# Kernel optimization log

Measured on AMD Instinct MI355X. Metric: run time of the kernel, lower is better.

Reference implementation:

```python
import jax, jax.numpy as jnp
import numpy as np

B, L, H = 32, 2048, 512
EPS = 1e-6


def setup_inputs() -> dict:
    key = jax.random.key(0)
    k1, k2 = jax.random.split(key)
    hidden = jax.random.normal(k1, (B, L, H), dtype=jnp.float32)
    # nn.Linear(H, H): weight [H, H], bias [H]; use kaiming-uniform-like scale
    bound = 1.0 / np.sqrt(H)
    W = jax.random.uniform(k2, (H, H), dtype=jnp.float32, minval=-bound, maxval=bound)
    b = jnp.zeros((H,), dtype=jnp.float32)
    return {"hidden": hidden, "W": W, "b": b}


def reference(hidden, W, b):
    Bn, Ln, Hn = hidden.shape

    def step(M, k):
        # k: [B, H]; key == value == hidden[:, t, :]
        v_pred = jnp.einsum("bij,bj->bi", M, k)               # M @ k
        denom = jnp.sum(k * k, axis=-1, keepdims=True) + EPS   # [B, 1]
        delta_v = k - v_pred / denom                           # v - v_pred/denom (v == k)
        M = M + jnp.einsum("bi,bj->bij", delta_v, k)           # outer-product update
        return M, None

    M0 = jnp.zeros((Bn, Hn, Hn), dtype=hidden.dtype)
    xs = jnp.swapaxes(hidden[:, :-1, :], 0, 1)  # [L-1, B, H]
    M, _ = jax.lax.scan(step, M0, xs)

    query = hidden[:, -1, :]                                   # [B, H]
    context = jnp.einsum("bij,bj->bi", M, query)               # [B, H]
    return context @ W.T + b                                   # read_proj
```

## Files before the change

### kernel.cpp

```cpp
#include <hip/hip_runtime.h>

#define B_  32
#define L_  2048
#define H_  512
#define T_  2047
#define CA  32
#define NC  64
#define EPSF 1e-6f

template <int CTRL>
__device__ __forceinline__ float dpp_shift_add(float x) {
  int t = __builtin_amdgcn_update_dpp(0, __float_as_int(x), CTRL, 0xf, 0xf, true);
  return x + __int_as_float(t);
}
__device__ __forceinline__ float wave_reduce_lane63(float x) {
  x = dpp_shift_add<0x111>(x);
  x = dpp_shift_add<0x112>(x);
  x = dpp_shift_add<0x114>(x);
  x = dpp_shift_add<0x118>(x);
  x = dpp_shift_add<0x142>(x);
  x = dpp_shift_add<0x143>(x);
  return x;
}

__device__ __forceinline__ void load_lds16(const float* g, float* l) {
  __builtin_amdgcn_global_load_lds(
      (const __attribute__((address_space(1))) unsigned int*)(g),
      (__attribute__((address_space(3))) unsigned int*)(l), 16, 0, 0);
}

__global__ __launch_bounds__(256) void
deltarule_gram(const float* __restrict__ hidden,
               float* __restrict__ tmT, float* __restrict__ dvec) {
  const int cb = blockIdx.x, b = blockIdx.y;
  const int tid = threadIdx.x, lane = tid & 63, wv = tid >> 6;
  __shared__ __align__(16) float Kc[CA * H_];
  __shared__ float G[CA * 33];

  const float* kb = hidden + ((size_t)b * L_ + (size_t)cb * CA) * H_;
#pragma unroll
  for (int u = 0; u < 16; ++u) {
    const int off = (u * 4 + wv) * 256;
    load_lds16(kb + off + 4 * lane, &Kc[off]);
  }
  __asm__ volatile("s_waitcnt vmcnt(0)" ::: "memory");
  __syncthreads();
  if (cb == NC - 1) {
    if (tid < 128) *(float4*)&Kc[31 * H_ + 4 * tid] = make_float4(0.f, 0.f, 0.f, 0.f);
    __syncthreads();
  }

  float kr[8][8];
#pragma unroll
  for (int i = 0; i < 8; ++i) {
    const int r = 8 * wv + i;
    *(float4*)&kr[i][0] = *(const float4*)&Kc[r * H_ + 4 * lane];
    *(float4*)&kr[i][4] = *(const float4*)&Kc[r * H_ + 256 + 4 * lane];
  }
  float g[8] = {0.f, 0.f, 0.f, 0.f, 0.f, 0.f, 0.f, 0.f};
  for (int j = 8 * wv; j < CA; ++j) {
    float kj[8];
    *(float4*)&kj[0] = *(const float4*)&Kc[j * H_ + 4 * lane];
    *(float4*)&kj[4] = *(const float4*)&Kc[j * H_ + 256 + 4 * lane];
#pragma unroll
    for (int i = 0; i < 8; ++i) {
      float p = kr[i][0] * kj[0];
#pragma unroll
      for (int u = 1; u < 8; ++u) p = fmaf(kr[i][u], kj[u], p);
      p = wave_reduce_lane63(p);
      float s = __int_as_float(__builtin_amdgcn_readlane(__float_as_int(p), 63));
      g[i] = (lane == j) ? s : g[i];
    }
  }
  if (lane < CA) {
#pragma unroll
    for (int i = 0; i < 8; ++i) G[(8 * wv + i) * 33 + lane] = g[i];
  }
  __syncthreads();

  if (wv == 0) {
    const int j = lane & 31;
    float X[CA];
#pragma unroll
    for (int t = CA - 1; t >= 0; --t) {
      float inner = 0.f;
#pragma unroll
      for (int s = t + 1; s < CA; ++s) inner = fmaf(G[t * 33 + s], X[s], inner);
      X[t] = (((j == t) ? 1.f : 0.f) - inner) / (G[t * 33 + t] + EPSF);
    }
    if (lane < CA) {
      const size_t base = ((size_t)b * NC + cb) * (CA * CA);
#pragma unroll
      for (int u = 0; u < 8; ++u)
        *(float4*)&tmT[base + j * CA + 4 * u] =
            make_float4(X[4 * u], X[4 * u + 1], X[4 * u + 2], X[4 * u + 3]);
      dvec[((size_t)b * NC + cb) * CA + lane] = G[j * 33 + j] + EPSF;
    }
  }
}

__global__ __launch_bounds__(512) void
deltarule_scan(const float* __restrict__ hidden,
               const float* __restrict__ Wm, const float* __restrict__ bias,
               const float* __restrict__ tmT, const float* __restrict__ dvec,
               float* __restrict__ out) {
  const int b = blockIdx.x, tid = threadIdx.x, lane = tid & 63, wv = tid >> 6;
  __shared__ __align__(16) float Kc[2][CA * H_];
  __shared__ float Tm[CA * 33];
  __shared__ float Dv[CA];
  __shared__ float Yv[CA];
  __shared__ float2 SigS[CA];
  __shared__ __align__(16) float Wv[H_];
  __shared__ __align__(16) float Ctx[H_];

  const float* hb = hidden + (size_t)b * L_ * H_;
  float wh = hb[(size_t)(L_ - 1) * H_ + tid];
  Wv[tid] = wh;
  float ch = 0.f;

  {
    const float* kb = hb + (size_t)(NC - 1) * CA * H_;
#pragma unroll
    for (int u = 0; u < 8; ++u) {
      const int off = (u * 8 + wv) * 256;
      load_lds16(kb + off + 4 * lane, &Kc[1][off]);
    }
    const size_t tb = (size_t)b * NC + (NC - 1);
    float2 t2 = *(const float2*)&tmT[tb * (CA * CA) + 2 * tid];
    const int e0 = 2 * tid;
    Tm[(e0 >> 5) * 33 + (e0 & 31)] = t2.x;
    Tm[((e0 + 1) >> 5) * 33 + ((e0 + 1) & 31)] = t2.y;
    if (tid < CA) Dv[tid] = dvec[tb * CA + tid];
  }
  __asm__ volatile("s_waitcnt vmcnt(0)" ::: "memory");
  __syncthreads();
  if (tid < 128) *(float4*)&Kc[1][31 * H_ + 4 * tid] = make_float4(0.f, 0.f, 0.f, 0.f);
  __syncthreads();

  for (int c = NC - 1; c >= 0; --c) {
    const int buf = c & 1;

    float2 tmN = make_float2(0.f, 0.f); float dN = 0.f;
    if (c > 0) {
      const size_t tb = (size_t)b * NC + (c - 1);
      tmN = *(const float2*)&tmT[tb * (CA * CA) + 2 * tid];
      if (tid < CA) dN = dvec[tb * CA + tid];
      const float* kb = hb + (size_t)(c - 1) * CA * H_;
#pragma unroll
      for (int u = 0; u < 8; ++u) {
        const int off = (u * 8 + wv) * 256;
        load_lds16(kb + off + 4 * lane, &Kc[buf ^ 1][off]);
      }
    }

    {
      float4 wa = *(const float4*)&Wv[4 * lane];
      float4 wb = *(const float4*)&Wv[256 + 4 * lane];
#pragma unroll
      for (int i = 0; i < 4; ++i) {
        const int r = 4 * wv + i;
        float4 ka = *(const float4*)&Kc[buf][r * H_ + 4 * lane];
        float4 kc = *(const float4*)&Kc[buf][r * H_ + 256 + 4 * lane];
        float p = ka.x * wa.x;
        p = fmaf(ka.y, wa.y, p); p = fmaf(ka.z, wa.z, p); p = fmaf(ka.w, wa.w, p);
        p = fmaf(kc.x, wb.x, p); p = fmaf(kc.y, wb.y, p);
        p = fmaf(kc.z, wb.z, p); p = fmaf(kc.w, wb.w, p);
        p = wave_reduce_lane63(p);
        if (lane == 63) Yv[r] = p;
      }
    }
    __syncthreads();

    if (wv == 0) {
      const int j = lane & 31, hf = lane >> 5;
      float sig = 0.f;
#pragma unroll
      for (int s0 = 0; s0 < 16; ++s0) {
        const int s = hf * 16 + s0;
        sig = fmaf(Tm[s * 33 + j], Yv[s], sig);
      }
      sig += __shfl_down(sig, 32);
      if (lane < CA) SigS[j] = make_float2(sig, Dv[j] * sig);
    }
    __syncthreads();

    if (c > 0) {
      const int e0 = 2 * tid;
      Tm[(e0 >> 5) * 33 + (e0 & 31)] = tmN.x;
      Tm[((e0 + 1) >> 5) * 33 + ((e0 + 1) & 31)] = tmN.y;
      if (tid < CA) Dv[tid] = dN;
    }

#pragma unroll
    for (int t = 0; t < CA; ++t) {
      float2 ss = SigS[t];
      float kvv = Kc[buf][t * H_ + tid];
      wh = fmaf(-ss.x, kvv, wh);
      ch = fmaf(ss.y, kvv, ch);
    }
    Wv[tid] = wh;
    __asm__ volatile("s_waitcnt vmcnt(0)" ::: "memory");
    __syncthreads();
  }

  Ctx[tid] = ch;
  __syncthreads();
  float acc = bias[tid];
  const float* wr = Wm + (size_t)tid * H_;
#pragma unroll 8
  for (int i = 0; i < H_; i += 4) {
    float4 w4 = *(const float4*)(wr + i);
    float4 cv = *(const float4*)&Ctx[i];
    acc = fmaf(w4.x, cv.x, acc); acc = fmaf(w4.y, cv.y, acc);
    acc = fmaf(w4.z, cv.z, acc); acc = fmaf(w4.w, cv.w, acc);
  }
  out[(size_t)b * H_ + tid] = acc;
}

extern "C" void kernel_launch(void* const* d_in, const int* in_sizes, int n_in,
                              void* d_out, int out_size, void* d_ws, size_t ws_size,
                              hipStream_t stream) {
  const float* hidden = (const float*)d_in[0];
  const float* Wm     = (const float*)d_in[1];
  const float* bias   = (const float*)d_in[2];
  float* out = (float*)d_out;

  float* tmT  = (float*)d_ws;
  float* dvec = tmT + (size_t)B_ * NC * CA * CA;

  dim3 gridA(NC, B_);
  deltarule_gram<<<gridA, 256, 0, stream>>>(hidden, tmT, dvec);
  deltarule_scan<<<B_, 512, 0, stream>>>(hidden, Wm, bias, tmT, dvec, out);
}
```

Measured before the change: 386.3 us.

## Stage keys as fp16 copy and triple-buffer the chunked delta-rule scan

```diff
diff --git a/kernel.cpp b/kernel.cpp
--- a/kernel.cpp
+++ b/kernel.cpp
@@ -1,4 +1,5 @@
 #include <hip/hip_runtime.h>
+#include <hip/hip_fp16.h>
 
 #define B_  32
 #define L_  2048
@@ -28,10 +29,16 @@
       (const __attribute__((address_space(1))) unsigned int*)(g),
       (__attribute__((address_space(3))) unsigned int*)(l), 16, 0, 0);
 }
+__device__ __forceinline__ void load_lds16h(const unsigned short* g, unsigned short* l) {
+  __builtin_amdgcn_global_load_lds(
+      (const __attribute__((address_space(1))) unsigned int*)(g),
+      (__attribute__((address_space(3))) unsigned int*)(l), 16, 0, 0);
+}
 
 __global__ __launch_bounds__(256) void
 deltarule_gram(const float* __restrict__ hidden,
-               float* __restrict__ tmT, float* __restrict__ dvec) {
+               float* __restrict__ tmT, float* __restrict__ dvec,
+               unsigned short* __restrict__ Kh) {
   const int cb = blockIdx.x, b = blockIdx.y;
   const int tid = threadIdx.x, lane = tid & 63, wv = tid >> 6;
   __shared__ __align__(16) float Kc[CA * H_];
@@ -47,6 +54,19 @@
   __syncthreads();
   if (cb == NC - 1) {
     if (tid < 128) *(float4*)&Kc[31 * H_ + 4 * tid] = make_float4(0.f, 0.f, 0.f, 0.f);
+    __syncthreads();
+  }
+
+  if (Kh) {
+    unsigned int* dst = (unsigned int*)(Kh + ((size_t)b * L_ + (size_t)cb * CA) * H_);
+#pragma unroll
+    for (int u = 0; u < 32; ++u) {
+      const int i = u * 256 + tid;
+      float2 v = *(const float2*)&Kc[2 * i];
+      __half2 h2 = __floats2half2_rn(v.x, v.y);
+      dst[i] = *(const unsigned int*)&h2;
+      *(float2*)&Kc[2 * i] = __half22float2(h2);
+    }
     __syncthreads();
   }
 
@@ -100,10 +120,150 @@
 }
 
 __global__ __launch_bounds__(512) void
-deltarule_scan(const float* __restrict__ hidden,
-               const float* __restrict__ Wm, const float* __restrict__ bias,
-               const float* __restrict__ tmT, const float* __restrict__ dvec,
-               float* __restrict__ out) {
+deltarule_scan_f16(const float* __restrict__ hidden,
+                   const unsigned short* __restrict__ Kh,
+                   const float* __restrict__ Wm, const float* __restrict__ bias,
+                   const float* __restrict__ tmT, const float* __restrict__ dvec,
+                   float* __restrict__ out) {
+  const int b = blockIdx.x, tid = threadIdx.x, lane = tid & 63, wv = tid >> 6;
+  __shared__ __align__(16) unsigned short Kc[3][CA * H_];
+  __shared__ float Tm[2][CA * 33];
+  __shared__ float Yv[CA];
+  __shared__ float2 SigS[CA];
+  __shared__ __align__(16) float Wv[H_];
+  __shared__ __align__(16) float Ctx[H_];
+
+  const float* hb = hidden + (size_t)b * L_ * H_;
+  const unsigned short* kbb = Kh + (size_t)b * L_ * H_;
+
+  float wh = hb[(size_t)(L_ - 1) * H_ + tid];
+  Wv[tid] = wh;
+  float ch = 0.f;
+
+  {
+    const unsigned short* kp = kbb + (size_t)(NC - 1) * CA * H_;
+#pragma unroll
+    for (int u = 0; u < 4; ++u) {
+      const int off = (u * 8 + wv) * 512;
+      load_lds16h(kp + off + 8 * lane, &Kc[(NC - 1) % 3][off]);
+    }
+  }
+  asm volatile("" ::: "memory");
+  const size_t tbP = (size_t)b * NC + (NC - 1);
+  float2 tmR = *(const float2*)&tmT[tbP * (CA * CA) + 2 * tid];
+  float dR = dvec[tbP * CA + (lane & 31)];
+  asm volatile("" ::: "memory");
+  {
+    const unsigned short* kp = kbb + (size_t)(NC - 2) * CA * H_;
+#pragma unroll
+    for (int u = 0; u < 4; ++u) {
+      const int off = (u * 8 + wv) * 512;
+      load_lds16h(kp + off + 8 * lane, &Kc[(NC - 2) % 3][off]);
+    }
+  }
+  asm volatile("" ::: "memory");
+  {
+    const int f0 = 2 * tid;
+    Tm[1][(f0 >> 5) * 33 + (f0 & 31)] = tmR.x;
+    Tm[1][((f0 + 1) >> 5) * 33 + ((f0 + 1) & 31)] = tmR.y;
+  }
+  float dCur = dR;
+  asm volatile("s_waitcnt vmcnt(4) lgkmcnt(0)\n\ts_barrier" ::: "memory");
+
+  for (int c = NC - 1; c >= 0; --c) {
+    const int rb = c % 3;
+
+    if (c >= 1) {
+      const size_t tb = (size_t)b * NC + (c - 1);
+      tmR = *(const float2*)&tmT[tb * (CA * CA) + 2 * tid];
+      dR = dvec[tb * CA + (lane & 31)];
+    }
+    asm volatile("" ::: "memory");
+    if (c >= 2) {
+      const unsigned short* kp = kbb + (size_t)(c - 2) * CA * H_;
+#pragma unroll
+      for (int u = 0; u < 4; ++u) {
+        const int off = (u * 8 + wv) * 512;
+        load_lds16h(kp + off + 8 * lane, &Kc[(c - 2) % 3][off]);
+      }
+    }
+    asm volatile("" ::: "memory");
+
+    {
+      float4 wa = *(const float4*)&Wv[8 * lane];
+      float4 wb2 = *(const float4*)&Wv[8 * lane + 4];
+#pragma unroll
+      for (int i = 0; i < 4; ++i) {
+        const int r = 4 * wv + i;
+        uint4 kw = *(const uint4*)&Kc[rb][r * H_ + 8 * lane];
+        float2 f0 = __half22float2(*(__half2*)&kw.x);
+        float2 f1 = __half22float2(*(__half2*)&kw.y);
+        float2 f2 = __half22float2(*(__half2*)&kw.z);
+        float2 f3 = __half22float2(*(__half2*)&kw.w);
+        float p = f0.x * wa.x;
+        p = fmaf(f0.y, wa.y, p); p = fmaf(f1.x, wa.z, p); p = fmaf(f1.y, wa.w, p);
+        p = fmaf(f2.x, wb2.x, p); p = fmaf(f2.y, wb2.y, p);
+        p = fmaf(f3.x, wb2.z, p); p = fmaf(f3.y, wb2.w, p);
+        p = wave_reduce_lane63(p);
+        if (lane == 63) Yv[r] = p;
+      }
+    }
+    asm volatile("s_waitcnt lgkmcnt(0)\n\ts_barrier" ::: "memory");
+
+    {
+      const int j = lane & 31, hf = lane >> 5;
+      float sig = 0.f;
+#pragma unroll
+      for (int s0 = 0; s0 < 16; ++s0) {
+        const int s = hf * 16 + s0;
+        sig = fmaf(Tm[c & 1][s * 33 + j], Yv[s], sig);
+      }
+      sig += __shfl_xor(sig, 32);
+      float sj = dCur * sig;
+      if (lane < 32) SigS[j] = make_float2(sig, sj);
+    }
+    if (c >= 1) {
+      const int f0 = 2 * tid;
+      Tm[(c - 1) & 1][(f0 >> 5) * 33 + (f0 & 31)] = tmR.x;
+      Tm[(c - 1) & 1][((f0 + 1) >> 5) * 33 + ((f0 + 1) & 31)] = tmR.y;
+      dCur = dR;
+    }
+
+#pragma unroll
+    for (int t = 0; t < CA; ++t) {
+      float2 ss = SigS[t];
+      float kvv = __half2float(*(const __half*)&Kc[rb][t * H_ + tid]);
+      wh = fmaf(-ss.x, kvv, wh);
+      ch = fmaf(ss.y, kvv, ch);
+    }
+    Wv[tid] = wh;
+
+    if (c >= 2) {
+      asm volatile("s_waitcnt vmcnt(4) lgkmcnt(0)\n\ts_barrier" ::: "memory");
+    } else {
+      asm volatile("s_waitcnt vmcnt(0) lgkmcnt(0)\n\ts_barrier" ::: "memory");
+    }
+  }
+
+  Ctx[tid] = ch;
+  __syncthreads();
+  float acc = bias[tid];
+  const float* wr = Wm + (size_t)tid * H_;
+#pragma unroll 8
+  for (int i = 0; i < H_; i += 4) {
+    float4 w4 = *(const float4*)(wr + i);
+    float4 cv = *(const float4*)&Ctx[i];
+    acc = fmaf(w4.x, cv.x, acc); acc = fmaf(w4.y, cv.y, acc);
+    acc = fmaf(w4.z, cv.z, acc); acc = fmaf(w4.w, cv.w, acc);
+  }
+  out[(size_t)b * H_ + tid] = acc;
+}
+
+__global__ __launch_bounds__(512) void
+deltarule_scan_f32(const float* __restrict__ hidden,
+                   const float* __restrict__ Wm, const float* __restrict__ bias,
+                   const float* __restrict__ tmT, const float* __restrict__ dvec,
+                   float* __restrict__ out) {
   const int b = blockIdx.x, tid = threadIdx.x, lane = tid & 63, wv = tid >> 6;
   __shared__ __align__(16) float Kc[2][CA * H_];
   __shared__ float Tm[CA * 33];
@@ -139,7 +299,6 @@
 
   for (int c = NC - 1; c >= 0; --c) {
     const int buf = c & 1;
-
     float2 tmN = make_float2(0.f, 0.f); float dN = 0.f;
     if (c > 0) {
       const size_t tb = (size_t)b * NC + (c - 1);
@@ -152,7 +311,6 @@
         load_lds16(kb + off + 4 * lane, &Kc[buf ^ 1][off]);
       }
     }
-
     {
       float4 wa = *(const float4*)&Wv[4 * lane];
       float4 wb = *(const float4*)&Wv[256 + 4 * lane];
@@ -170,7 +328,6 @@
       }
     }
     __syncthreads();
-
     if (wv == 0) {
       const int j = lane & 31, hf = lane >> 5;
       float sig = 0.f;
@@ -183,14 +340,12 @@
       if (lane < CA) SigS[j] = make_float2(sig, Dv[j] * sig);
     }
     __syncthreads();
-
     if (c > 0) {
       const int e0 = 2 * tid;
       Tm[(e0 >> 5) * 33 + (e0 & 31)] = tmN.x;
       Tm[((e0 + 1) >> 5) * 33 + ((e0 + 1) & 31)] = tmN.y;
       if (tid < CA) Dv[tid] = dN;
     }
-
 #pragma unroll
     for (int t = 0; t < CA; ++t) {
       float2 ss = SigS[t];
@@ -225,10 +380,21 @@
   const float* bias   = (const float*)d_in[2];
   float* out = (float*)d_out;
 
-  float* tmT  = (float*)d_ws;
-  float* dvec = tmT + (size_t)B_ * NC * CA * CA;
+  const size_t szKh = (size_t)B_ * L_ * H_ * sizeof(unsigned short);
+  const size_t szTm = (size_t)B_ * NC * CA * CA * sizeof(float);
+  const size_t szD  = (size_t)B_ * NC * CA * sizeof(float);
 
   dim3 gridA(NC, B_);
-  deltarule_gram<<<gridA, 256, 0, stream>>>(hidden, tmT, dvec);
-  deltarule_scan<<<B_, 512, 0, stream>>>(hidden, Wm, bias, tmT, dvec, out);
-}
+  if (ws_size >= szKh + szTm + szD) {
+    unsigned short* Kh = (unsigned short*)d_ws;
+    float* tmT  = (float*)((char*)d_ws + szKh);
+    float* dvec = tmT + (size_t)B_ * NC * CA * CA;
+    deltarule_gram<<<gridA, 256, 0, stream>>>(hidden, tmT, dvec, Kh);
+    deltarule_scan_f16<<<B_, 512, 0, stream>>>(hidden, Kh, Wm, bias, tmT, dvec, out);
+  } else {
+    float* tmT  = (float*)d_ws;
+    float* dvec = tmT + (size_t)B_ * NC * CA * CA;
+    deltarule_gram<<<gridA, 256, 0, stream>>>(hidden, tmT, dvec, nullptr);
+    deltarule_scan_f32<<<B_, 512, 0, stream>>>(hidden, Wm, bias, tmT, dvec, out);
+  }
+}
```

Result: slower. 399.2 us (+3.3%).
